# Optimization experiments

Hardware: AMD Instinct MI355X
Metric: run time of the kernel (lower is better)

Reference implementation:

```python
import jax, jax.numpy as jnp
import numpy as np

N, C, HW = 32, 256, 64          # batch, in_channels, input_size
K = 128                          # n_clusters
S = 8                            # blocks per side
BLOCK = (HW + S - 1) // S        # = 8, padding_size = 0


def setup_inputs() -> dict:
    key = jax.random.key(0)
    k1, k2 = jax.random.split(key)
    x = jax.random.normal(k1, (N, C, HW, HW), dtype=jnp.float32)
    cluster_centers = jax.random.normal(k2, (K, C), dtype=jnp.float32)
    return {"x": x, "cluster_centers": cluster_centers}


def reference(x, cluster_centers):
    # --- Codebook: argmin over squared distances, computed without the
    x2 = jnp.sum(x * x, axis=1)                       # (N, H, W)
    c2 = jnp.sum(cluster_centers * cluster_centers, axis=1)  # (K,)
    xc = jnp.einsum('nchw,kc->nkhw', x, cluster_centers)     # (N, K, H, W)
    dist = x2[:, None] - 2.0 * xc + c2[None, :, None, None]
    code = jnp.argmin(dist, axis=1)                   # (N, H, W) int

    # --- BlockWiseHistogramEncoder: unfold into S*S non-overlapping
    # BLOCKxBLOCK blocks (padding_size == 0 here), one_hot(code+1), mean ---
    shifted = code + 1                                # values in [1, K]
    n = shifted.shape[0]
    blocks = shifted.reshape(n, S, BLOCK, S, BLOCK)
    blocks = blocks.transpose(0, 1, 3, 2, 4).reshape(n, S * S, BLOCK * BLOCK)
    onehot = (blocks[..., None] == jnp.arange(K + 1)).astype(jnp.float32)
    return onehot.mean(axis=2)                        # (N, S*S, K+1)
```

## Files before the change

### kernel.cpp

```cpp
#include <hip/hip_runtime.h>

#define C_DIM 256
#define K_DIM 128
#define HW_DIM 64
#define PIX 4096
#define N_IMG 32

using short8 = __attribute__((ext_vector_type(8))) short;
using f32x4  = __attribute__((ext_vector_type(4))) float;

__device__ __forceinline__ void lds_barrier() {
    asm volatile("s_waitcnt lgkmcnt(0)\n\ts_barrier" ::: "memory");
}

__device__ __forceinline__ unsigned long long umin64(unsigned long long a, unsigned long long b) {
    return a < b ? a : b;
}
__device__ __forceinline__ unsigned mono(float d) {
    unsigned u = __float_as_uint(d);
    return u ^ ((u & 0x80000000u) ? 0xFFFFFFFFu : 0x80000000u);
}

__device__ __forceinline__ void split3t(float v, unsigned& hu, unsigned& mu, unsigned& lu) {
    unsigned u = __float_as_uint(v);
    unsigned hf = u & 0xffff0000u;
    float r1 = v - __uint_as_float(hf);
    unsigned r1u = __float_as_uint(r1);
    unsigned mf = r1u & 0xffff0000u;
    float r2 = r1 - __uint_as_float(mf);
    hu = u; mu = r1u; lu = __float_as_uint(r2);
}

__global__ __launch_bounds__(64) void prep_kernel(const float* __restrict__ cl,
                                                  unsigned short* __restrict__ Bt,
                                                  float* __restrict__ c2) {
    int k = blockIdx.x;
    int lane = threadIdx.x;
    const float4* row = (const float4*)(cl + k * C_DIM);
    float4 v = row[lane];
    float vv[4] = {v.x, v.y, v.z, v.w};
    unsigned short* bk = Bt + k * 768 + lane * 4;
#pragma unroll
    for (int i = 0; i < 4; ++i) {
        unsigned hu, mu, lu;
        split3t(vv[i], hu, mu, lu);
        bk[i]       = (unsigned short)(hu >> 16);
        bk[256 + i] = (unsigned short)(mu >> 16);
        bk[512 + i] = (unsigned short)(lu >> 16);
    }
    if (lane == 0) {
        float s = 0.f;
#pragma unroll
        for (int i = 0; i < C_DIM / 4; ++i) {
            float4 u = row[i];
            s = fmaf(u.x, u.x, s);
            s = fmaf(u.y, u.y, s);
            s = fmaf(u.z, u.z, s);
            s = fmaf(u.w, u.w, s);
        }
        c2[k] = s;
    }
}

__global__ __launch_bounds__(256, 4) void main_kernel(
    const float* __restrict__ x, const unsigned short* __restrict__ Bt,
    const float* __restrict__ c2v, unsigned char* __restrict__ code) {

    __shared__ __align__(16) unsigned short Ap[3 * 4096];
    __shared__ float x2p[2][128];
    unsigned long long* red = (unsigned long long*)Ap;

    const int t    = threadIdx.x;
    const int lane = t & 63;
    const int w    = t >> 6;
    const int q    = lane >> 4;
    const int l15  = lane & 15;

    const int px = t & 127;
    const int h  = t >> 7;

    const int b   = blockIdx.x;
    const int img = b >> 5;
    const int pb  = (b & 31) * 128;

    const float* xg = x + (size_t)img * (C_DIM * PIX) + pb + px;

    f32x4 acc[8][2];
#pragma unroll
    for (int m = 0; m < 8; ++m)
#pragma unroll
        for (int ns = 0; ns < 2; ++ns) acc[m][ns] = (f32x4){0.f, 0.f, 0.f, 0.f};

    float xr[16];
#pragma unroll
    for (int j = 0; j < 16; ++j) xr[j] = xg[(size_t)(h * 16 + j) * PIX];

    float x2part = 0.f;
    const unsigned short* btb = Bt + (w * 32 + l15) * 768 + q * 8;

    const int wbase = (px >> 4) * 512 + (px & 15) * 8 + h * 2 * 128;

#pragma unroll 1
    for (int ci = 0; ci < 8; ++ci) {
#pragma unroll
        for (int g = 0; g < 2; ++g) {
            unsigned p0[4], p1[4], p2[4];
#pragma unroll
            for (int jj = 0; jj < 4; ++jj) {
                float v0 = xr[g * 8 + jj * 2], v1 = xr[g * 8 + jj * 2 + 1];
                unsigned h0, m0, l0, h1, m1, l1;
                split3t(v0, h0, m0, l0);
                split3t(v1, h1, m1, l1);
                p0[jj] = (h0 >> 16) | (h1 & 0xffff0000u);
                p1[jj] = (m0 >> 16) | (m1 & 0xffff0000u);
                p2[jj] = (l0 >> 16) | (l1 & 0xffff0000u);
                x2part = fmaf(v0, v0, x2part);
                x2part = fmaf(v1, v1, x2part);
            }
            int base = wbase + g * 128;
            *(uint4*)&Ap[base]            = make_uint4(p0[0], p0[1], p0[2], p0[3]);
            *(uint4*)&Ap[4096 + base]     = make_uint4(p1[0], p1[1], p1[2], p1[3]);
            *(uint4*)&Ap[8192 + base]     = make_uint4(p2[0], p2[1], p2[2], p2[3]);
        }
        if (ci == 7) x2p[h][px] = x2part;

        short8 bv[3][2];
#pragma unroll
        for (int p = 0; p < 3; ++p) {
            bv[p][0] = *(const short8*)(btb + p * 256 + ci * 32);
            bv[p][1] = *(const short8*)(btb + 16 * 768 + p * 256 + ci * 32);
        }

        if (ci < 7) {
#pragma unroll
            for (int j = 0; j < 16; ++j)
                xr[j] = xg[(size_t)((ci + 1) * 32 + h * 16 + j) * PIX];
        }

        lds_barrier();

#pragma unroll
        for (int pa = 0; pa < 3; ++pa) {
#pragma unroll
            for (int mg = 0; mg < 4; ++mg) {
                const int m0 = mg * 2, m1 = mg * 2 + 1;
                short8 af0 = *(const short8*)&Ap[pa * 4096 + m0 * 512 + lane * 8];
                short8 af1 = *(const short8*)&Ap[pa * 4096 + m1 * 512 + lane * 8];
#pragma unroll
                for (int pb2 = 0; pb2 < 3; ++pb2) {
                    if (pb2 < 3 - pa) {
                        acc[m0][0] = __builtin_amdgcn_mfma_f32_16x16x32_bf16(af0, bv[pb2][0], acc[m0][0], 0, 0, 0);
                        acc[m0][1] = __builtin_amdgcn_mfma_f32_16x16x32_bf16(af0, bv[pb2][1], acc[m0][1], 0, 0, 0);
                        acc[m1][0] = __builtin_amdgcn_mfma_f32_16x16x32_bf16(af1, bv[pb2][0], acc[m1][0], 0, 0, 0);
                        acc[m1][1] = __builtin_amdgcn_mfma_f32_16x16x32_bf16(af1, bv[pb2][1], acc[m1][1], 0, 0, 0);
                    }
                }
            }
        }
        lds_barrier();
    }

    const float c2a0 = c2v[w * 32 + l15];
    const float c2a1 = c2v[w * 32 + 16 + l15];
    const unsigned n0 = (unsigned)(w * 32 + l15);
    const unsigned n1 = n0 + 16;

#pragma unroll
    for (int m = 0; m < 8; ++m) {
#pragma unroll
        for (int r = 0; r < 4; ++r) {
            int pxl = m * 16 + q * 4 + r;
            float x2v = x2p[0][pxl] + x2p[1][pxl];
            float d0 = (x2v - 2.0f * acc[m][0][r]) + c2a0;
            float d1 = (x2v - 2.0f * acc[m][1][r]) + c2a1;
            unsigned long long k0 = ((unsigned long long)mono(d0) << 32) | n0;
            unsigned long long k1 = ((unsigned long long)mono(d1) << 32) | n1;
            unsigned long long best = umin64(k0, k1);
            best = umin64(best, __shfl_xor(best, 1));
            best = umin64(best, __shfl_xor(best, 2));
            best = umin64(best, __shfl_xor(best, 4));
            best = umin64(best, __shfl_xor(best, 8));
            if (l15 == 0) red[w * 128 + pxl] = best;
        }
    }
    lds_barrier();

    if (t < 128) {
        unsigned long long m0 = umin64(umin64(red[t], red[128 + t]),
                                       umin64(red[256 + t], red[384 + t]));
        code[(size_t)img * PIX + pb + t] = (unsigned char)(m0 & 0xFFu);
    }
}

__global__ __launch_bounds__(256) void hist_kernel(const unsigned char* __restrict__ code,
                                                   float* __restrict__ out) {
    __shared__ int hist[4][K_DIM + 1];
    int wid = threadIdx.x >> 6, lane = threadIdx.x & 63;
    int b = blockIdx.x * 4 + wid;
    int n = b >> 6, sy = (b >> 3) & 7, sx = b & 7;

    hist[wid][lane] = 0;
    hist[wid][lane + 64] = 0;
    if (lane == 0) hist[wid][128] = 0;
    __syncthreads();

    int hh = sy * 8 + (lane >> 3);
    int ww = sx * 8 + (lane & 7);
    int c = code[n * PIX + hh * HW_DIM + ww];
    atomicAdd(&hist[wid][c + 1], 1);
    __syncthreads();

    const float inv = 1.0f / 64.0f;
    out[(size_t)b * (K_DIM + 1) + lane] = hist[wid][lane] * inv;
    out[(size_t)b * (K_DIM + 1) + 64 + lane] = hist[wid][lane + 64] * inv;
    if (lane == 0) out[(size_t)b * (K_DIM + 1) + 128] = hist[wid][128] * inv;
}

extern "C" void kernel_launch(void* const* d_in, const int* in_sizes, int n_in,
                              void* d_out, int out_size, void* d_ws, size_t ws_size,
                              hipStream_t stream) {
    const float* x  = (const float*)d_in[0];
    const float* cl = (const float*)d_in[1];
    float* out = (float*)d_out;

    unsigned short* Bt = (unsigned short*)d_ws;
    float* c2 = (float*)((char*)d_ws + 196608);
    unsigned char* code = (unsigned char*)d_ws + 197120;

    prep_kernel<<<K_DIM, 64, 0, stream>>>(cl, Bt, c2);
    main_kernel<<<(N_IMG * PIX) / 128, 256, 0, stream>>>(x, Bt, c2, code);
    hist_kernel<<<(N_IMG * 64) / 4, 256, 0, stream>>>(code, out);
}
```

Measured before the change: 217.0 us.

## Make each wave own its own pixels across all clusters, removing block barriers

Work is re-split so each wavefront handles 32 pixels against all 128 clusters, instead of the whole block sharing 128 pixels with each wave covering 32 clusters. The A tiles live in a per-wave LDS slice, so both per-iteration block barriers and the final cross-wave LDS argmin reduction go away; the argmin now finishes inside the wave with shuffles. In exchange each wave loads the full split-bf16 codebook slice from global/L1 every channel chunk, which is four times more B loads per wave. It also keeps 16 accumulator tiles in registers, now laid out 2x8 instead of 8x2.

```diff
diff --git a/kernel.cpp b/kernel.cpp
--- a/kernel.cpp
+++ b/kernel.cpp
@@ -8,10 +8,6 @@
 
 using short8 = __attribute__((ext_vector_type(8))) short;
 using f32x4  = __attribute__((ext_vector_type(4))) float;
-
-__device__ __forceinline__ void lds_barrier() {
-    asm volatile("s_waitcnt lgkmcnt(0)\n\ts_barrier" ::: "memory");
-}
 
 __device__ __forceinline__ unsigned long long umin64(unsigned long long a, unsigned long long b) {
     return a < b ? a : b;
@@ -66,9 +62,8 @@
     const float* __restrict__ x, const unsigned short* __restrict__ Bt,
     const float* __restrict__ c2v, unsigned char* __restrict__ code) {
 
-    __shared__ __align__(16) unsigned short Ap[3 * 4096];
-    __shared__ float x2p[2][128];
-    unsigned long long* red = (unsigned long long*)Ap;
+    __shared__ __align__(16) unsigned short Aw[4][3072];
+    __shared__ float x2w[4][32];
 
     const int t    = threadIdx.x;
     const int lane = t & 63;
@@ -76,29 +71,30 @@
     const int q    = lane >> 4;
     const int l15  = lane & 15;
 
-    const int px = t & 127;
-    const int h  = t >> 7;
+    const int pxl  = lane & 31;
+    const int h    = lane >> 5;
 
     const int b   = blockIdx.x;
     const int img = b >> 5;
     const int pb  = (b & 31) * 128;
-
-    const float* xg = x + (size_t)img * (C_DIM * PIX) + pb + px;
-
-    f32x4 acc[8][2];
-#pragma unroll
-    for (int m = 0; m < 8; ++m)
-#pragma unroll
-        for (int ns = 0; ns < 2; ++ns) acc[m][ns] = (f32x4){0.f, 0.f, 0.f, 0.f};
+    const int wpx = pb + w * 32;
+
+    const float* xg = x + (size_t)img * (C_DIM * PIX) + wpx + pxl;
+    const unsigned short* btv = Bt + l15 * 768 + q * 8;
+
+    f32x4 acc[2][8];
+#pragma unroll
+    for (int m = 0; m < 2; ++m)
+#pragma unroll
+        for (int kg = 0; kg < 8; ++kg) acc[m][kg] = (f32x4){0.f, 0.f, 0.f, 0.f};
 
     float xr[16];
 #pragma unroll
     for (int j = 0; j < 16; ++j) xr[j] = xg[(size_t)(h * 16 + j) * PIX];
 
     float x2part = 0.f;
-    const unsigned short* btb = Bt + (w * 32 + l15) * 768 + q * 8;
-
-    const int wbase = (px >> 4) * 512 + (px & 15) * 8 + h * 2 * 128;
+    unsigned short* aw = Aw[w];
+    const int wbase = (pxl >> 4) * 512 + (pxl & 15) * 8 + h * 256;
 
 #pragma unroll 1
     for (int ci = 0; ci < 8; ++ci) {
@@ -118,17 +114,16 @@
                 x2part = fmaf(v1, v1, x2part);
             }
             int base = wbase + g * 128;
-            *(uint4*)&Ap[base]            = make_uint4(p0[0], p0[1], p0[2], p0[3]);
-            *(uint4*)&Ap[4096 + base]     = make_uint4(p1[0], p1[1], p1[2], p1[3]);
-            *(uint4*)&Ap[8192 + base]     = make_uint4(p2[0], p2[1], p2[2], p2[3]);
-        }
-        if (ci == 7) x2p[h][px] = x2part;
-
-        short8 bv[3][2];
-#pragma unroll
-        for (int p = 0; p < 3; ++p) {
-            bv[p][0] = *(const short8*)(btb + p * 256 + ci * 32);
-            bv[p][1] = *(const short8*)(btb + 16 * 768 + p * 256 + ci * 32);
+            *(uint4*)&aw[base]        = make_uint4(p0[0], p0[1], p0[2], p0[3]);
+            *(uint4*)&aw[1024 + base] = make_uint4(p1[0], p1[1], p1[2], p1[3]);
+            *(uint4*)&aw[2048 + base] = make_uint4(p2[0], p2[1], p2[2], p2[3]);
+        }
+
+        short8 af[3][2];
+#pragma unroll
+        for (int pa = 0; pa < 3; ++pa) {
+            af[pa][0] = *(const short8*)&aw[pa * 1024 + lane * 8];
+            af[pa][1] = *(const short8*)&aw[pa * 1024 + 512 + lane * 8];
         }
 
         if (ci < 7) {
@@ -137,58 +132,57 @@
                 xr[j] = xg[(size_t)((ci + 1) * 32 + h * 16 + j) * PIX];
         }
 
-        lds_barrier();
-
-#pragma unroll
-        for (int pa = 0; pa < 3; ++pa) {
-#pragma unroll
-            for (int mg = 0; mg < 4; ++mg) {
-                const int m0 = mg * 2, m1 = mg * 2 + 1;
-                short8 af0 = *(const short8*)&Ap[pa * 4096 + m0 * 512 + lane * 8];
-                short8 af1 = *(const short8*)&Ap[pa * 4096 + m1 * 512 + lane * 8];
-#pragma unroll
-                for (int pb2 = 0; pb2 < 3; ++pb2) {
-                    if (pb2 < 3 - pa) {
-                        acc[m0][0] = __builtin_amdgcn_mfma_f32_16x16x32_bf16(af0, bv[pb2][0], acc[m0][0], 0, 0, 0);
-                        acc[m0][1] = __builtin_amdgcn_mfma_f32_16x16x32_bf16(af0, bv[pb2][1], acc[m0][1], 0, 0, 0);
-                        acc[m1][0] = __builtin_amdgcn_mfma_f32_16x16x32_bf16(af1, bv[pb2][0], acc[m1][0], 0, 0, 0);
-                        acc[m1][1] = __builtin_amdgcn_mfma_f32_16x16x32_bf16(af1, bv[pb2][1], acc[m1][1], 0, 0, 0);
-                    }
-                }
+#pragma unroll
+        for (int kg = 0; kg < 8; ++kg) {
+            const unsigned short* bb = btv + kg * 12288 + ci * 32;
+            short8 bv0 = *(const short8*)(bb);
+            short8 bv1 = *(const short8*)(bb + 256);
+            short8 bv2 = *(const short8*)(bb + 512);
+            acc[0][kg] = __builtin_amdgcn_mfma_f32_16x16x32_bf16(af[0][0], bv0, acc[0][kg], 0, 0, 0);
+            acc[1][kg] = __builtin_amdgcn_mfma_f32_16x16x32_bf16(af[0][1], bv0, acc[1][kg], 0, 0, 0);
+            acc[0][kg] = __builtin_amdgcn_mfma_f32_16x16x32_bf16(af[0][0], bv1, acc[0][kg], 0, 0, 0);
+            acc[1][kg] = __builtin_amdgcn_mfma_f32_16x16x32_bf16(af[0][1], bv1, acc[1][kg], 0, 0, 0);
+            acc[0][kg] = __builtin_amdgcn_mfma_f32_16x16x32_bf16(af[0][0], bv2, acc[0][kg], 0, 0, 0);
+            acc[1][kg] = __builtin_amdgcn_mfma_f32_16x16x32_bf16(af[0][1], bv2, acc[1][kg], 0, 0, 0);
+            acc[0][kg] = __builtin_amdgcn_mfma_f32_16x16x32_bf16(af[1][0], bv0, acc[0][kg], 0, 0, 0);
+            acc[1][kg] = __builtin_amdgcn_mfma_f32_16x16x32_bf16(af[1][1], bv0, acc[1][kg], 0, 0, 0);
+            acc[0][kg] = __builtin_amdgcn_mfma_f32_16x16x32_bf16(af[1][0], bv1, acc[0][kg], 0, 0, 0);
+            acc[1][kg] = __builtin_amdgcn_mfma_f32_16x16x32_bf16(af[1][1], bv1, acc[1][kg], 0, 0, 0);
+            acc[0][kg] = __builtin_amdgcn_mfma_f32_16x16x32_bf16(af[2][0], bv0, acc[0][kg], 0, 0, 0);
+            acc[1][kg] = __builtin_amdgcn_mfma_f32_16x16x32_bf16(af[2][1], bv0, acc[1][kg], 0, 0, 0);
+        }
+    }
+
+    float x2o = __shfl_xor(x2part, 32);
+    float x2tot = x2part + x2o;
+    if (lane < 32) x2w[w][pxl] = x2tot;
+
+    float c2r[8];
+#pragma unroll
+    for (int kg = 0; kg < 8; ++kg) c2r[kg] = c2v[kg * 16 + l15];
+
+    const int g4 = (lane >> 4) * 4;
+    const size_t cb = (size_t)img * PIX + wpx;
+
+#pragma unroll
+    for (int m = 0; m < 2; ++m) {
+#pragma unroll
+        for (int r = 0; r < 4; ++r) {
+            float x2v = x2w[w][m * 16 + g4 + r];
+            unsigned long long best = 0xFFFFFFFFFFFFFFFFull;
+#pragma unroll
+            for (int kg = 0; kg < 8; ++kg) {
+                float d = (x2v - 2.0f * acc[m][kg][r]) + c2r[kg];
+                unsigned long long key =
+                    ((unsigned long long)mono(d) << 32) | (unsigned)(kg * 16 + l15);
+                best = umin64(best, key);
             }
-        }
-        lds_barrier();
-    }
-
-    const float c2a0 = c2v[w * 32 + l15];
-    const float c2a1 = c2v[w * 32 + 16 + l15];
-    const unsigned n0 = (unsigned)(w * 32 + l15);
-    const unsigned n1 = n0 + 16;
-
-#pragma unroll
-    for (int m = 0; m < 8; ++m) {
-#pragma unroll
-        for (int r = 0; r < 4; ++r) {
-            int pxl = m * 16 + q * 4 + r;
-            float x2v = x2p[0][pxl] + x2p[1][pxl];
-            float d0 = (x2v - 2.0f * acc[m][0][r]) + c2a0;
-            float d1 = (x2v - 2.0f * acc[m][1][r]) + c2a1;
-            unsigned long long k0 = ((unsigned long long)mono(d0) << 32) | n0;
-            unsigned long long k1 = ((unsigned long long)mono(d1) << 32) | n1;
-            unsigned long long best = umin64(k0, k1);
             best = umin64(best, __shfl_xor(best, 1));
             best = umin64(best, __shfl_xor(best, 2));
             best = umin64(best, __shfl_xor(best, 4));
             best = umin64(best, __shfl_xor(best, 8));
-            if (l15 == 0) red[w * 128 + pxl] = best;
-        }
-    }
-    lds_barrier();
-
-    if (t < 128) {
-        unsigned long long m0 = umin64(umin64(red[t], red[128 + t]),
-                                       umin64(red[256 + t], red[384 + t]));
-        code[(size_t)img * PIX + pb + t] = (unsigned char)(m0 & 0xFFu);
+            if (l15 == 0) code[cb + m * 16 + g4 + r] = (unsigned char)(best & 0xFFu);
+        }
     }
 }
 
```

After: 275.7 us. 1.27x slower.
